# Kernel tuning notes

Hardware: AMD Instinct MI355X
Metric: run time of the kernel (lower is better)

## Reference

```python
import jax, jax.numpy as jnp
import numpy as np

D_MODEL, HEADS, D_FF = 1024, 16, 4096
D_K = D_MODEL // HEADS
EPS = 1e-5


def layer_norm(x, g, b):
    mu = jnp.mean(x, axis=-1, keepdims=True)
    var = jnp.mean((x - mu) ** 2, axis=-1, keepdims=True)
    return (x - mu) * jax.lax.rsqrt(var + EPS) * g + b


def setup_inputs() -> dict:
    key = jax.random.key(0)
    ks = jax.random.split(key, 16)
    B, S = 2, 2048
    s = 0.02
    return {
        "src": jax.random.normal(ks[0], (B, S, D_MODEL), jnp.float32),
        "corr": jax.random.normal(ks[1], (B, S, S), jnp.float32),
        "pos": jax.random.normal(ks[2], (B, S, D_MODEL), jnp.float32),
        "Wq": jax.random.normal(ks[3], (D_MODEL, D_MODEL), jnp.float32) * s,
        "bq": jnp.zeros((D_MODEL,), jnp.float32),
        "Wk": jax.random.normal(ks[4], (D_MODEL, D_MODEL), jnp.float32) * s,
        "bk": jnp.zeros((D_MODEL,), jnp.float32),
        "Wv": jax.random.normal(ks[5], (D_MODEL, D_MODEL), jnp.float32) * s,
        "bv": jnp.zeros((D_MODEL,), jnp.float32),
        "Wo": jax.random.normal(ks[6], (D_MODEL, D_MODEL), jnp.float32) * s,
        "bo": jnp.zeros((D_MODEL,), jnp.float32),
        "W1": jax.random.normal(ks[7], (D_MODEL, D_FF), jnp.float32) * s,
        "b1": jnp.zeros((D_FF,), jnp.float32),
        "W2": jax.random.normal(ks[8], (D_FF, D_MODEL), jnp.float32) * s,
        "b2": jnp.zeros((D_MODEL,), jnp.float32),
        "g1": jnp.ones((D_MODEL,), jnp.float32),
        "be1": jnp.zeros((D_MODEL,), jnp.float32),
        "g2": jnp.ones((D_MODEL,), jnp.float32),
        "be2": jnp.zeros((D_MODEL,), jnp.float32),
    }


def reference(src, corr, pos, Wq, bq, Wk, bk, Wv, bv, Wo, bo, W1, b1, W2, b2, g1, be1, g2, be2):
    B, S, _ = src.shape
    qk_in = src + pos  # with_pos_embed for q and k; value uses raw src
    # QKV projections -> [B, H, S, d_k]
    def split_heads(x):
        return x.reshape(B, S, HEADS, D_K).transpose(0, 2, 1, 3)
    q = split_heads(qk_in @ Wq + bq)
    k = split_heads(qk_in @ Wk + bk)
    v = split_heads(src @ Wv + bv)
    # scores [B, H, S, S] with additive correlation bias before softmax
    scores = jnp.einsum("bhqd,bhkd->bhqk", q, k) / jnp.sqrt(jnp.float32(D_K))
    scores = scores + corr[:, None, :, :]
    attn = jax.nn.softmax(scores, axis=-1)
    ctx = jnp.einsum("bhqk,bhkd->bhqd", attn, v)
    concat = ctx.transpose(0, 2, 1, 3).reshape(B, S, D_MODEL)
    attn_out = concat @ Wo + bo
    # post-norm residual blocks (dropout = identity in eval)
    x = layer_norm(src + attn_out, g1, be1)
    ffn = jax.nn.relu(x @ W1 + b1) @ W2 + b2
    x = layer_norm(x + ffn, g2, be2)
    return x
```

## Files before the change

### kernel.cpp

```cpp
#include <hip/hip_runtime.h>
#include <hip/hip_bf16.h>

#define S_LEN  2048
#define BATCH  2
#define DMODEL 1024
#define NHEAD  16
#define DHEAD  64
#define DFF    4096
#define NTOK   (BATCH * S_LEN)
#define QKVLD  3072

typedef __attribute__((ext_vector_type(8))) short short8;
typedef __attribute__((ext_vector_type(4))) short short4v;
typedef __attribute__((ext_vector_type(4))) float f32x4;

__device__ __forceinline__ short f2bs(float f) {
  __hip_bfloat16 h = __float2bfloat16(f);
  short s;
  __builtin_memcpy(&s, &h, sizeof(short));
  return s;
}

__device__ __forceinline__ float bs2f(short s) {
  unsigned u = ((unsigned)(unsigned short)s) << 16;
  float f;
  __builtin_memcpy(&f, &u, sizeof(float));
  return f;
}

__device__ __forceinline__ f32x4 mfma16(short8 a, short8 b, f32x4 c) {
  return __builtin_amdgcn_mfma_f32_16x16x32_bf16(a, b, c, 0, 0, 0);
}

__device__ __forceinline__ void load_lds16(const short* g, short* l) {
  __builtin_amdgcn_global_load_lds(
      (const __attribute__((address_space(1))) void*)g,
      (__attribute__((address_space(3))) void*)l, 16, 0, 0);
}

__global__ void prep_static(
    const float* __restrict__ Wq, const float* __restrict__ Wk,
    const float* __restrict__ Wv, const float* __restrict__ Wo,
    const float* __restrict__ W1, const float* __restrict__ W2,
    const float* __restrict__ bq, const float* __restrict__ bk,
    const float* __restrict__ bv,
    short* __restrict__ WqkvT, short* __restrict__ WoT,
    short* __restrict__ W1T, short* __restrict__ W2T,
    float* __restrict__ bqkv) {
  const int gid = blockIdx.x;
  const int tx = threadIdx.x, ty = threadIdx.y;

  if (gid >= 12288) {
    const int i = (gid - 12288) * 256 + ty * 32 + tx;
    float v;
    if (i < DMODEL) v = bq[i] * 0.125f;
    else if (i < 2 * DMODEL) v = bk[i - DMODEL];
    else v = bv[i - 2 * DMODEL];
    bqkv[i] = v;
    return;
  }

  const float* in;
  short* out;
  int R, C, t;
  float scale = 1.0f;
  if (gid < 4096) {
    t = gid & 1023;
    R = C = 1024;
    if (gid < 1024)      { in = Wq; out = WqkvT;                 scale = 0.125f; }
    else if (gid < 2048) { in = Wk; out = WqkvT + 1024 * 1024; }
    else if (gid < 3072) { in = Wv; out = WqkvT + 2 * 1024 * 1024; }
    else                 { in = Wo; out = WoT; }
  } else if (gid < 8192) {
    t = gid - 4096; in = W1; out = W1T; R = 1024; C = 4096;
  } else {
    t = gid - 8192; in = W2; out = W2T; R = 4096; C = 1024;
  }
  const int tpr = C >> 5;
  const int c0 = (t % tpr) * 32, r0 = (t / tpr) * 32;

  __shared__ float tile[32][33];
#pragma unroll
  for (int i = 0; i < 32; i += 8)
    tile[ty + i][tx] = in[(size_t)(r0 + ty + i) * C + c0 + tx];
  __syncthreads();
#pragma unroll
  for (int i = 0; i < 32; i += 8)
    out[(size_t)(c0 + ty + i) * R + r0 + tx] = f2bs(tile[tx][ty + i] * scale);
}

__global__ void prep_inputs(const float* __restrict__ src, const float* __restrict__ pos,
                            const float* __restrict__ corr,
                            short* __restrict__ qkb, short* __restrict__ srcb,
                            short* __restrict__ corrb) {
  const int gid = blockIdx.x;
  if (gid < 4096) {
    const int i = gid * 1024 + threadIdx.x * 4;
    float4 s = *(const float4*)(src + i);
    float4 p = *(const float4*)(pos + i);
    short4v q4 = {f2bs(s.x + p.x), f2bs(s.y + p.y), f2bs(s.z + p.z), f2bs(s.w + p.w)};
    short4v s4 = {f2bs(s.x), f2bs(s.y), f2bs(s.z), f2bs(s.w)};
    *(short4v*)(qkb + i) = q4;
    *(short4v*)(srcb + i) = s4;
  } else {
    const size_t i = ((size_t)(gid - 4096)) * 1024 + threadIdx.x * 4;
    float4 c = *(const float4*)(corr + i);
    short4v o = {f2bs(c.x), f2bs(c.y), f2bs(c.z), f2bs(c.w)};
    *(short4v*)(corrb + i) = o;
  }
}

__global__ __launch_bounds__(256) void transpose_bf16(
    const short* __restrict__ in, short* __restrict__ out, int R, int LDin) {
  __shared__ __attribute__((aligned(16))) short tile[64][72];
  const int c0 = blockIdx.x * 64, r0 = blockIdx.y * 64;
#pragma unroll
  for (int i = 0; i < 2; i++) {
    const int idx = threadIdx.x + 256 * i;
    const int rr = idx >> 3, cc8 = (idx & 7) * 8;
    *(int4*)(&tile[rr][cc8]) = *(const int4*)(in + (size_t)(r0 + rr) * LDin + c0 + cc8);
  }
  __syncthreads();
#pragma unroll
  for (int i = 0; i < 2; i++) {
    const int idx = threadIdx.x + 256 * i;
    const int rr = idx >> 3, cc8 = (idx & 7) * 8;
    short8 v;
#pragma unroll
    for (int j = 0; j < 8; j++) v[j] = tile[cc8 + j][rr];
    *(short8*)(out + (size_t)(c0 + rr) * R + r0 + cc8) = v;
  }
}

template <int RELU, int OUT_BF16>
__global__ __launch_bounds__(256) void gemm_bt(
    const short* __restrict__ A0, const short* __restrict__ A1,
    const short* __restrict__ Bt, const float* __restrict__ bias,
    float* __restrict__ Cf, short* __restrict__ Cb,
    int M, int N, int K, int splitcol) {
  __shared__ __attribute__((aligned(16))) short As[128 * 32];
  __shared__ __attribute__((aligned(16))) short Bs[128 * 32];

  const int tid = threadIdx.x;
  const int wave = tid >> 6, lane = tid & 63;
  const int lm = lane & 15, lq = lane >> 4;
  const int row0 = blockIdx.y * 128, col0 = blockIdx.x * 128;
  const int wr = (wave >> 1) * 64, wc = (wave & 1) * 64;

  const short* A = (col0 < splitcol) ? A0 : A1;
  const short* ag = A + (size_t)(row0 + wave * 32 + (lane >> 2)) * K + (lane & 3) * 8;
  const short* bg = Bt + (size_t)(col0 + wave * 32 + (lane >> 2)) * K + (lane & 3) * 8;
  short* asl = &As[wave * 32 * 32];
  short* bsl = &Bs[wave * 32 * 32];

  f32x4 acc[4][4];
#pragma unroll
  for (int i = 0; i < 4; i++)
#pragma unroll
    for (int j = 0; j < 4; j++) acc[i][j] = (f32x4){0.f, 0.f, 0.f, 0.f};

  for (int k0 = 0; k0 < K; k0 += 32) {
    load_lds16(ag + k0, asl);
    load_lds16(ag + (size_t)16 * K + k0, asl + 16 * 32);
    load_lds16(bg + k0, bsl);
    load_lds16(bg + (size_t)16 * K + k0, bsl + 16 * 32);
    __syncthreads();

    short8 af[4], bfr[4];
#pragma unroll
    for (int i = 0; i < 4; i++)
      af[i] = *(const short8*)(&As[(wr + 16 * i + lm) * 32 + lq * 8]);
#pragma unroll
    for (int j = 0; j < 4; j++)
      bfr[j] = *(const short8*)(&Bs[(wc + 16 * j + lm) * 32 + lq * 8]);
#pragma unroll
    for (int i = 0; i < 4; i++)
#pragma unroll
      for (int j = 0; j < 4; j++) acc[i][j] = mfma16(af[i], bfr[j], acc[i][j]);
    __syncthreads();
  }

#pragma unroll
  for (int i = 0; i < 4; i++) {
#pragma unroll
    for (int j = 0; j < 4; j++) {
      const int col = col0 + wc + 16 * j + lm;
      const float bs = bias[col];
#pragma unroll
      for (int r = 0; r < 4; r++) {
        const int row = row0 + wr + 16 * i + lq * 4 + r;
        float v = acc[i][j][r] + bs;
        if (RELU) v = fmaxf(v, 0.f);
        if (OUT_BF16)
          Cb[(size_t)row * N + col] = f2bs(v);
        else
          Cf[(size_t)row * N + col] = v;
      }
    }
  }
}

__global__ __launch_bounds__(256) void gemm_bt_part(
    const short* __restrict__ A, const short* __restrict__ Bt,
    float* __restrict__ Cf, int M, int N, int K, int Kslice) {
  __shared__ __attribute__((aligned(16))) short As[128 * 32];
  __shared__ __attribute__((aligned(16))) short Bs[128 * 32];

  const int tid = threadIdx.x;
  const int wave = tid >> 6, lane = tid & 63;
  const int lm = lane & 15, lq = lane >> 4;
  const int row0 = blockIdx.y * 128, col0 = blockIdx.x * 128;
  const int kbase = blockIdx.z * Kslice;
  const int wr = (wave >> 1) * 64, wc = (wave & 1) * 64;
  Cf += (size_t)blockIdx.z * M * N;

  const short* ag = A + (size_t)(row0 + wave * 32 + (lane >> 2)) * K + (lane & 3) * 8;
  const short* bg = Bt + (size_t)(col0 + wave * 32 + (lane >> 2)) * K + (lane & 3) * 8;
  short* asl = &As[wave * 32 * 32];
  short* bsl = &Bs[wave * 32 * 32];

  f32x4 acc[4][4];
#pragma unroll
  for (int i = 0; i < 4; i++)
#pragma unroll
    for (int j = 0; j < 4; j++) acc[i][j] = (f32x4){0.f, 0.f, 0.f, 0.f};

  for (int k0 = kbase; k0 < kbase + Kslice; k0 += 32) {
    load_lds16(ag + k0, asl);
    load_lds16(ag + (size_t)16 * K + k0, asl + 16 * 32);
    load_lds16(bg + k0, bsl);
    load_lds16(bg + (size_t)16 * K + k0, bsl + 16 * 32);
    __syncthreads();

    short8 af[4], bfr[4];
#pragma unroll
    for (int i = 0; i < 4; i++)
      af[i] = *(const short8*)(&As[(wr + 16 * i + lm) * 32 + lq * 8]);
#pragma unroll
    for (int j = 0; j < 4; j++)
      bfr[j] = *(const short8*)(&Bs[(wc + 16 * j + lm) * 32 + lq * 8]);
#pragma unroll
    for (int i = 0; i < 4; i++)
#pragma unroll
      for (int j = 0; j < 4; j++) acc[i][j] = mfma16(af[i], bfr[j], acc[i][j]);
    __syncthreads();
  }

#pragma unroll
  for (int i = 0; i < 4; i++) {
#pragma unroll
    for (int j = 0; j < 4; j++) {
      const int col = col0 + wc + 16 * j + lm;
#pragma unroll
      for (int r = 0; r < 4; r++) {
        const int row = row0 + wr + 16 * i + lq * 4 + r;
        Cf[(size_t)row * N + col] = acc[i][j][r];
      }
    }
  }
}

__global__ __launch_bounds__(512, 8) void attn_kernel(
    const short* __restrict__ QKV,
    const short* __restrict__ VT,
    const short* __restrict__ corrb,
    short* __restrict__ ctx) {
  const int h = blockIdx.x, qtile = blockIdx.y;
  const int b = blockIdx.z;
  const int tid = threadIdx.x;
  const int wave = tid >> 6, lane = tid & 63;
  const int lm = lane & 15, lq = lane >> 4;
  const int qb = qtile * 128 + wave * 16;
  const int fx = lm & 7;
  const int fy = (lm >> 1) & 3;

  __shared__ __attribute__((aligned(16))) short Ks[32 * 64];
  __shared__ __attribute__((aligned(16))) short Vs[64 * 32];
  __shared__ __attribute__((aligned(16))) short Ps[8 * 16 * 32];

  const short* q0 = QKV + (size_t)(b * S_LEN + qb + lm) * QKVLD + h * DHEAD;
  const short8 qA0 = *(const short8*)(q0 + lq * 8);
  const short8 qA1 = *(const short8*)(q0 + lq * 8 + 32);

  f32x4 oA[4];
#pragma unroll
  for (int t = 0; t < 4; t++) oA[t] = (f32x4){0.f, 0.f, 0.f, 0.f};
  f32x4 lacc = (f32x4){0.f, 0.f, 0.f, 0.f};

  const short* c0 = corrb + (size_t)(b * S_LEN + qb + lm) * S_LEN;

  const int st = tid & 255;
  const bool isK = tid < 256;
  short* sdst;
  const short* sgp;
  size_t sstep;
  if (isK) {
    const int krow = st >> 3, ku = st & 7;
    sdst = &Ks[krow * 64 + ((ku ^ (krow & 7)) * 8)];
    sgp = QKV + (size_t)(b * S_LEN + krow) * QKVLD + DMODEL + h * DHEAD + ku * 8;
    sstep = (size_t)32 * QKVLD;
  } else {
    const int vrow = st >> 2, vu = st & 3;
    sdst = &Vs[vrow * 32 + ((vu ^ ((vrow >> 1) & 3)) * 8)];
    sgp = VT + (size_t)(h * DHEAD + vrow) * NTOK + b * S_LEN + vu * 8;
    sstep = 32;
  }

  for (int kt = 0; kt < S_LEN; kt += 32) {
    *(int4*)sdst = *(const int4*)sgp;
    sgp += sstep;
    __syncthreads();

    f32x4 sv[2];
    __builtin_amdgcn_s_setprio(1);
#pragma unroll
    for (int t = 0; t < 2; t++) {
      const int rb = (t * 16 + lm) * 64;
      const short8 kf0 = *(const short8*)(&Ks[rb + (lq ^ fx) * 8]);
      const short8 kf1 = *(const short8*)(&Ks[rb + ((lq + 4) ^ fx) * 8]);
      f32x4 a = (f32x4){0.f, 0.f, 0.f, 0.f};
      a = mfma16(kf0, qA0, a);
      a = mfma16(kf1, qA1, a);
      sv[t] = a;
    }
    __builtin_amdgcn_s_setprio(0);

#pragma unroll
    for (int t = 0; t < 2; t++) {
      const short4v cr = *(const short4v*)(c0 + kt + t * 16 + lq * 4);
#pragma unroll
      for (int r = 0; r < 4; r++)
        sv[t][r] = __expf(sv[t][r] + bs2f(cr[r]));
      lacc += sv[t];
      short4v pA = {f2bs(sv[t][0]), f2bs(sv[t][1]), f2bs(sv[t][2]), f2bs(sv[t][3])};
      const int pu = ((2 * t + (lq >> 1)) ^ fy) * 8 + (lq & 1) * 4;
      *(short4v*)(&Ps[wave * 512 + lm * 32 + pu]) = pA;
    }

    const short8 pA0 = *(const short8*)(&Ps[wave * 512 + lm * 32 + (lq ^ fy) * 8]);
    __builtin_amdgcn_s_setprio(1);
#pragma unroll
    for (int t = 0; t < 4; t++) {
      const int vrb = (t * 16 + lm) * 32;
      const short8 vf0 = *(const short8*)(&Vs[vrb + (lq ^ fy) * 8]);
      oA[t] = mfma16(vf0, pA0, oA[t]);
    }
    __builtin_amdgcn_s_setprio(0);
    __syncthreads();
  }

  float lA = lacc[0] + lacc[1] + lacc[2] + lacc[3];
  lA += __shfl_xor(lA, 16);
  lA += __shfl_xor(lA, 32);
  const float inv = 1.0f / lA;
  short* op = ctx + (size_t)(b * S_LEN + qb + lm) * DMODEL + h * DHEAD;
#pragma unroll
  for (int t = 0; t < 4; t++) {
    short4v ov = {f2bs(oA[t][0] * inv), f2bs(oA[t][1] * inv),
                  f2bs(oA[t][2] * inv), f2bs(oA[t][3] * inv)};
    *(short4v*)(op + t * 16 + lq * 4) = ov;
  }
}

__global__ __launch_bounds__(256) void residual_ln3(
    const float* __restrict__ xa, const float* __restrict__ p0,
    const float* __restrict__ p1, const float* __restrict__ bias,
    const float* __restrict__ g, const float* __restrict__ be,
    float* __restrict__ outf, short* __restrict__ outb) {
  const int row = blockIdx.x;
  const int t = threadIdx.x;
  const size_t base = (size_t)row * DMODEL + t * 4;
  float4 a = *(const float4*)(xa + base);
  f32x4 q0 = *(const f32x4*)(p0 + base);
  f32x4 q1 = *(const f32x4*)(p1 + base);
  f32x4 bb = *(const f32x4*)(bias + t * 4);
  const float v0 = a.x + q0[0] + q1[0] + bb[0];
  const float v1 = a.y + q0[1] + q1[1] + bb[1];
  const float v2 = a.z + q0[2] + q1[2] + bb[2];
  const float v3 = a.w + q0[3] + q1[3] + bb[3];
  float sum = v0 + v1 + v2 + v3;
  float sq = v0 * v0 + v1 * v1 + v2 * v2 + v3 * v3;
#pragma unroll
  for (int off = 1; off < 64; off <<= 1) {
    sum += __shfl_xor(sum, off);
    sq += __shfl_xor(sq, off);
  }
  __shared__ float ssum[4], ssq[4];
  const int wave = t >> 6;
  if ((t & 63) == 0) { ssum[wave] = sum; ssq[wave] = sq; }
  __syncthreads();
  sum = ssum[0] + ssum[1] + ssum[2] + ssum[3];
  sq = ssq[0] + ssq[1] + ssq[2] + ssq[3];
  const float mean = sum * (1.0f / DMODEL);
  const float var = sq * (1.0f / DMODEL) - mean * mean;
  const float rstd = rsqrtf(var + 1e-5f);
  float4 gv = *(const float4*)(g + t * 4);
  float4 bv = *(const float4*)(be + t * 4);
  const float o0 = (v0 - mean) * rstd * gv.x + bv.x;
  const float o1 = (v1 - mean) * rstd * gv.y + bv.y;
  const float o2 = (v2 - mean) * rstd * gv.z + bv.z;
  const float o3 = (v3 - mean) * rstd * gv.w + bv.w;
  if (outf) {
    float4 ov = {o0, o1, o2, o3};
    *(float4*)(outf + base) = ov;
  }
  if (outb) {
    short4v ob = {f2bs(o0), f2bs(o1), f2bs(o2), f2bs(o3)};
    *(short4v*)(outb + base) = ob;
  }
}

extern "C" void kernel_launch(void* const* d_in, const int* in_sizes, int n_in,
                              void* d_out, int out_size, void* d_ws, size_t ws_size,
                              hipStream_t stream) {
  const float* src = (const float*)d_in[0];
  const float* corr = (const float*)d_in[1];
  const float* pos = (const float*)d_in[2];
  const float* Wq = (const float*)d_in[3];
  const float* bq = (const float*)d_in[4];
  const float* Wk = (const float*)d_in[5];
  const float* bk = (const float*)d_in[6];
  const float* Wv = (const float*)d_in[7];
  const float* bv = (const float*)d_in[8];
  const float* Wo = (const float*)d_in[9];
  const float* bo = (const float*)d_in[10];
  const float* W1 = (const float*)d_in[11];
  const float* b1 = (const float*)d_in[12];
  const float* W2 = (const float*)d_in[13];
  const float* b2 = (const float*)d_in[14];
  const float* g1 = (const float*)d_in[15];
  const float* be1 = (const float*)d_in[16];
  const float* g2 = (const float*)d_in[17];
  const float* be2 = (const float*)d_in[18];
  float* out = (float*)d_out;

  char* ws = (char*)d_ws;
  size_t off = 0;
  auto alloc = [&](size_t bytes) {
    char* p = ws + off;
    off += (bytes + 255) & ~(size_t)255;
    return p;
  };
  short* WqkvT = (short*)alloc((size_t)QKVLD * DMODEL * 2);
  short* WoT = (short*)alloc((size_t)DMODEL * DMODEL * 2);
  short* W1T = (short*)alloc((size_t)DFF * DMODEL * 2);
  short* W2T = (short*)alloc((size_t)DMODEL * DFF * 2);
  float* bqkv = (float*)alloc((size_t)QKVLD * 4);
  short* qkb = (short*)alloc((size_t)NTOK * DMODEL * 2);
  short* srcb = (short*)alloc((size_t)NTOK * DMODEL * 2);
  short* QKVb = (short*)alloc((size_t)NTOK * QKVLD * 2);
  short* VTt = (short*)alloc((size_t)DMODEL * NTOK * 2);
  short* corrb = (short*)alloc((size_t)BATCH * S_LEN * S_LEN * 2);
  short* ctxb = (short*)alloc((size_t)NTOK * DMODEL * 2);
  float* Pp = (float*)alloc((size_t)2 * NTOK * DMODEL * 4);
  short* Hb = (short*)alloc((size_t)NTOK * DFF * 2);
  float* x1f = (float*)alloc((size_t)NTOK * DMODEL * 4);
  short* x1b = (short*)alloc((size_t)NTOK * DMODEL * 2);

  prep_static<<<12300, dim3(32, 8), 0, stream>>>(
      Wq, Wk, Wv, Wo, W1, W2, bq, bk, bv, WqkvT, WoT, W1T, W2T, bqkv);

  prep_inputs<<<12288, 256, 0, stream>>>(src, pos, corr, qkb, srcb, corrb);

  gemm_bt<0, 1><<<dim3(QKVLD / 128, NTOK / 128), 256, 0, stream>>>(
      qkb, srcb, WqkvT, bqkv, nullptr, QKVb, NTOK, QKVLD, DMODEL, 2048);

  transpose_bf16<<<dim3(DMODEL / 64, NTOK / 64), 256, 0, stream>>>(
      QKVb + 2048, VTt, NTOK, QKVLD);

  attn_kernel<<<dim3(NHEAD, S_LEN / 128, BATCH), 512, 0, stream>>>(
      QKVb, VTt, corrb, ctxb);

  gemm_bt_part<<<dim3(DMODEL / 128, NTOK / 128, 2), 256, 0, stream>>>(
      ctxb, WoT, Pp, NTOK, DMODEL, DMODEL, DMODEL / 2);

  residual_ln3<<<NTOK, 256, 0, stream>>>(src, Pp, Pp + (size_t)NTOK * DMODEL,
                                         bo, g1, be1, x1f, x1b);

  gemm_bt<1, 1><<<dim3(DFF / 128, NTOK / 128), 256, 0, stream>>>(
      x1b, x1b, W1T, b1, nullptr, Hb, NTOK, DFF, DMODEL, 1 << 30);

  gemm_bt_part<<<dim3(DMODEL / 128, NTOK / 128, 2), 256, 0, stream>>>(
      Hb, W2T, Pp, NTOK, DMODEL, DFF, DFF / 2);

  residual_ln3<<<NTOK, 256, 0, stream>>>(x1f, Pp, Pp + (size_t)NTOK * DMODEL,
                                         b2, g2, be2, out, nullptr);
}
```

Baseline: 480.6 us.

## Split attention over key halves with smaller query tiles and a combine pass

The attention kernel now splits the key sequence into two halves. Each block handles 64 queries with 4 waves instead of 128 with 8, and writes unnormalized fp32 partial outputs and row sums into a scratch buffer. A new combine kernel adds the partials, normalizes them and writes the bf16 context. The aim is a finer-grained grid with better load balance across CUs, paid for with more K/V reloads per query, fp32 partial traffic and an extra launch.

```diff
diff --git a/kernel.cpp b/kernel.cpp
--- a/kernel.cpp
+++ b/kernel.cpp
@@ -9,6 +9,7 @@
 #define DFF    4096
 #define NTOK   (BATCH * S_LEN)
 #define QKVLD  3072
+#define NSPLIT 2
 
 typedef __attribute__((ext_vector_type(8))) short short8;
 typedef __attribute__((ext_vector_type(4))) short short4v;
@@ -260,23 +261,25 @@
   }
 }
 
-__global__ __launch_bounds__(512, 8) void attn_kernel(
+__global__ __launch_bounds__(256, 8) void attn_kernel(
     const short* __restrict__ QKV,
     const short* __restrict__ VT,
     const short* __restrict__ corrb,
-    short* __restrict__ ctx) {
+    float* __restrict__ Op,
+    float* __restrict__ lp) {
   const int h = blockIdx.x, qtile = blockIdx.y;
-  const int b = blockIdx.z;
+  const int b = blockIdx.z >> 1, split = blockIdx.z & 1;
+  const int koff = split * (S_LEN / NSPLIT);
   const int tid = threadIdx.x;
   const int wave = tid >> 6, lane = tid & 63;
   const int lm = lane & 15, lq = lane >> 4;
-  const int qb = qtile * 128 + wave * 16;
+  const int qb = qtile * 64 + wave * 16;
   const int fx = lm & 7;
   const int fy = (lm >> 1) & 3;
 
   __shared__ __attribute__((aligned(16))) short Ks[32 * 64];
   __shared__ __attribute__((aligned(16))) short Vs[64 * 32];
-  __shared__ __attribute__((aligned(16))) short Ps[8 * 16 * 32];
+  __shared__ __attribute__((aligned(16))) short Ps[4 * 16 * 32];
 
   const short* q0 = QKV + (size_t)(b * S_LEN + qb + lm) * QKVLD + h * DHEAD;
   const short8 qA0 = *(const short8*)(q0 + lq * 8);
@@ -289,26 +292,19 @@
 
   const short* c0 = corrb + (size_t)(b * S_LEN + qb + lm) * S_LEN;
 
-  const int st = tid & 255;
-  const bool isK = tid < 256;
-  short* sdst;
-  const short* sgp;
-  size_t sstep;
-  if (isK) {
-    const int krow = st >> 3, ku = st & 7;
-    sdst = &Ks[krow * 64 + ((ku ^ (krow & 7)) * 8)];
-    sgp = QKV + (size_t)(b * S_LEN + krow) * QKVLD + DMODEL + h * DHEAD + ku * 8;
-    sstep = (size_t)32 * QKVLD;
-  } else {
-    const int vrow = st >> 2, vu = st & 3;
-    sdst = &Vs[vrow * 32 + ((vu ^ ((vrow >> 1) & 3)) * 8)];
-    sgp = VT + (size_t)(h * DHEAD + vrow) * NTOK + b * S_LEN + vu * 8;
-    sstep = 32;
-  }
-
-  for (int kt = 0; kt < S_LEN; kt += 32) {
-    *(int4*)sdst = *(const int4*)sgp;
-    sgp += sstep;
+  const int krow = tid >> 3, ku = tid & 7;
+  short* kdst = &Ks[krow * 64 + ((ku ^ (krow & 7)) * 8)];
+  const short* kgp = QKV + (size_t)(b * S_LEN + koff + krow) * QKVLD + DMODEL +
+                     h * DHEAD + ku * 8;
+  const int vrow = tid >> 2, vu = tid & 3;
+  short* vdst = &Vs[vrow * 32 + ((vu ^ ((vrow >> 1) & 3)) * 8)];
+  const short* vgp = VT + (size_t)(h * DHEAD + vrow) * NTOK + b * S_LEN + koff + vu * 8;
+
+  for (int kt = koff; kt < koff + S_LEN / NSPLIT; kt += 32) {
+    *(int4*)kdst = *(const int4*)kgp;
+    *(int4*)vdst = *(const int4*)vgp;
+    kgp += (size_t)32 * QKVLD;
+    vgp += 32;
     __syncthreads();
 
     f32x4 sv[2];
@@ -352,14 +348,33 @@
   float lA = lacc[0] + lacc[1] + lacc[2] + lacc[3];
   lA += __shfl_xor(lA, 16);
   lA += __shfl_xor(lA, 32);
-  const float inv = 1.0f / lA;
-  short* op = ctx + (size_t)(b * S_LEN + qb + lm) * DMODEL + h * DHEAD;
-#pragma unroll
-  for (int t = 0; t < 4; t++) {
-    short4v ov = {f2bs(oA[t][0] * inv), f2bs(oA[t][1] * inv),
-                  f2bs(oA[t][2] * inv), f2bs(oA[t][3] * inv)};
-    *(short4v*)(op + t * 16 + lq * 4) = ov;
-  }
+  if (lq == 0)
+    lp[((size_t)split * NTOK + b * S_LEN + qb + lm) * NHEAD + h] = lA;
+  float* opA = Op + (size_t)split * NTOK * DMODEL +
+               (size_t)(b * S_LEN + qb + lm) * DMODEL + h * DHEAD;
+#pragma unroll
+  for (int t = 0; t < 4; t++)
+    *(f32x4*)(opA + t * 16 + lq * 4) = oA[t];
+}
+
+__global__ __launch_bounds__(256) void combine_ctx(
+    const float* __restrict__ Op, const float* __restrict__ lp,
+    short* __restrict__ ctx) {
+  const size_t idx = ((size_t)blockIdx.x * 256 + threadIdx.x) * 4;
+  const int token = (int)(idx >> 10);
+  const int d = (int)(idx & 1023);
+  const int h = d >> 6;
+  f32x4 o = (f32x4){0.f, 0.f, 0.f, 0.f};
+  float l = 0.f;
+#pragma unroll
+  for (int s = 0; s < NSPLIT; s++) {
+    o += *(const f32x4*)(Op + (size_t)s * NTOK * DMODEL + idx);
+    l += lp[((size_t)s * NTOK + token) * NHEAD + h];
+  }
+  const float inv = 1.0f / l;
+  short4v ov = {f2bs(o[0] * inv), f2bs(o[1] * inv),
+                f2bs(o[2] * inv), f2bs(o[3] * inv)};
+  *(short4v*)(ctx + idx) = ov;
 }
 
 __global__ __launch_bounds__(256) void residual_ln3(
@@ -452,8 +467,10 @@
   short* VTt = (short*)alloc((size_t)DMODEL * NTOK * 2);
   short* corrb = (short*)alloc((size_t)BATCH * S_LEN * S_LEN * 2);
   short* ctxb = (short*)alloc((size_t)NTOK * DMODEL * 2);
+  float* lp = (float*)alloc((size_t)NSPLIT * NTOK * NHEAD * 4);
   float* Pp = (float*)alloc((size_t)2 * NTOK * DMODEL * 4);
   short* Hb = (short*)alloc((size_t)NTOK * DFF * 2);
+  float* Op = Pp;
   float* x1f = (float*)alloc((size_t)NTOK * DMODEL * 4);
   short* x1b = (short*)alloc((size_t)NTOK * DMODEL * 2);
 
@@ -468,8 +485,9 @@
   transpose_bf16<<<dim3(DMODEL / 64, NTOK / 64), 256, 0, stream>>>(
       QKVb + 2048, VTt, NTOK, QKVLD);
 
-  attn_kernel<<<dim3(NHEAD, S_LEN / 128, BATCH), 512, 0, stream>>>(
-      QKVb, VTt, corrb, ctxb);
+  attn_kernel<<<dim3(NHEAD, S_LEN / 64, BATCH * NSPLIT), 256, 0, stream>>>(
+      QKVb, VTt, corrb, Op, lp);
+  combine_ctx<<<(NTOK * DMODEL) / (256 * 4), 256, 0, stream>>>(Op, lp, ctxb);
 
   gemm_bt_part<<<dim3(DMODEL / 128, NTOK / 128, 2), 256, 0, stream>>>(
       ctxb, WoT, Pp, NTOK, DMODEL, DMODEL, DMODEL / 2);
```

Result: no change. 478.2 us (-0.5%).
